# Kernel tuning notes

Measured on AMD Instinct MI355X. Metric: run time of the kernel, lower is better.

The kernel has to match this reference:

```python
import jax, jax.numpy as jnp
import numpy as np

N = 100000   # nodes
E = 1600000  # edges
F = 128      # num_features
NF = 4       # n_factor
D = 64       # n_dim = dim // n_factor = 256 // 4
NL = 3       # n_layer
G = 128      # num graphs in batch


def setup_inputs() -> dict:
    key = jax.random.key(0)
    ks = jax.random.split(key, 10)
    s = 0.05
    x = jax.random.normal(ks[0], (N, F), jnp.float32)
    edge_index = jax.random.randint(ks[1], (2, E), 0, N)
    att = jax.random.uniform(ks[2], (NF, E), jnp.float32)
    batch = jnp.sort(jax.random.randint(ks[3], (N,), 0, G))
    lin_W = jax.random.normal(ks[4], (NF, F, D), jnp.float32) * s
    lin_b = jnp.zeros((NF, D), jnp.float32)
    conv_Wrel = jax.random.normal(ks[5], (NF, NL, D, D), jnp.float32) * s
    conv_brel = jnp.zeros((NF, NL, D), jnp.float32)
    conv_Wroot = jax.random.normal(ks[6], (NF, NL, D, D), jnp.float32) * s
    gru_Wih = jax.random.normal(ks[7], (NF, 3 * D, D), jnp.float32) * s
    gru_Whh = jax.random.normal(ks[8], (NF, 3 * D, D), jnp.float32) * s
    gru_bih = jnp.zeros((NF, 3 * D), jnp.float32)
    gru_bhh = jnp.zeros((NF, 3 * D), jnp.float32)
    return dict(x=x, edge_index=edge_index, att=att, batch=batch,
                lin_W=lin_W, lin_b=lin_b,
                conv_Wrel=conv_Wrel, conv_brel=conv_brel, conv_Wroot=conv_Wroot,
                gru_Wih=gru_Wih, gru_Whh=gru_Whh, gru_bih=gru_bih, gru_bhh=gru_bhh,
                num_graphs=G)


def _gru_cell(xin, h, Wih, Whh, bih, bhh):
    # torch.nn.GRU single step: r,z,n gates
    gi = xin @ Wih.T + bih  # [N, 3D]
    gh = h @ Whh.T + bhh
    ir, iz, inn = jnp.split(gi, 3, axis=-1)
    hr, hz, hn = jnp.split(gh, 3, axis=-1)
    r = jax.nn.sigmoid(ir + hr)
    z = jax.nn.sigmoid(iz + hz)
    n = jnp.tanh(inn + r * hn)
    return (1.0 - z) * n + z * h


def reference(x, edge_index, att, batch, lin_W, lin_b, conv_Wrel, conv_brel,
              conv_Wroot, gru_Wih, gru_Whh, gru_bih, gru_bhh, num_graphs):
    src, dst = edge_index[0], edge_index[1]
    counts = jax.ops.segment_sum(jnp.ones((N,), x.dtype), batch, num_segments=num_graphs)
    counts = jnp.maximum(counts, 1.0)[:, None]
    outs, feats = [], []
    for f in range(NF):
        w = att[f][:, None]                       # [E,1] edge weights for this factor
        out = x @ lin_W[f] + lin_b[f]             # [N,D]
        h = out                                   # initial GRU hidden state
        for l in range(NL):
            # GraphConv: lin_rel(scatter_add(w * x_src -> dst)) + lin_root(x)
            agg = jax.ops.segment_sum(out[src] * w, dst, num_segments=N)
            m = jax.nn.relu(agg @ conv_Wrel[f, l] + conv_brel[f, l] + out @ conv_Wroot[f, l])
            h = _gru_cell(m, h, gru_Wih[f], gru_Whh[f], gru_bih[f], gru_bhh[f])
            out = h
        feats.append(out)
        # global mean pool
        outs.append(jax.ops.segment_sum(out, batch, num_segments=num_graphs) / counts)
    return (jnp.stack(outs), jnp.stack(feats))
```

## Files before the change

### kernel.cpp

```cpp
#include <hip/hip_runtime.h>

#define NN   100000
#define EE   1600000
#define FDIM 128
#define NFAC 4
#define DD   64
#define NLAY 3
#define GG   128
#define ROW  (NFAC * DD)

#define PF_STRIDE 57344
#define OFF_WREL  8192
#define OFF_WROOT 20480
#define OFF_WIH   32768
#define OFF_WHH   45056
#define PREP_TOTAL (NFAC * PF_STRIDE)

typedef __bf16 bf16x8_t __attribute__((ext_vector_type(8)));
typedef float  f32x4_t  __attribute__((ext_vector_type(4)));

__device__ __forceinline__ unsigned short f2bf(float x) {
    unsigned u = __float_as_uint(x);
    u += 0x7fffu + ((u >> 16) & 1u);
    return (unsigned short)(u >> 16);
}
__device__ __forceinline__ float b2f(unsigned short h) {
    return __uint_as_float(((unsigned)h) << 16);
}
__device__ __forceinline__ float sigm(float x) { return 1.f / (1.f + __expf(-x)); }
__device__ __forceinline__ float tanh_f(float x) {
    float t = __expf(-2.f * fabsf(x));
    float r = (1.f - t) / (1.f + t);
    return x >= 0.f ? r : -r;
}

__global__ __launch_bounds__(256) void k_init(int* deg, int* cursor, float* outs) {
    int i = blockIdx.x * 256 + threadIdx.x;
    if (i < NN) { deg[i] = 0; cursor[i] = 0; }
    if (i < NFAC * GG * DD) outs[i] = 0.f;
}

__global__ __launch_bounds__(256) void k_prep(const float* x, const float* linW,
                                              const float* wrel, const float* wroot,
                                              const float* wih, const float* whh,
                                              unsigned short* x16, unsigned short* prep) {
    for (int i = blockIdx.x * 256 + threadIdx.x; i < NN * FDIM; i += gridDim.x * 256)
        x16[i] = f2bf(x[i]);
    for (int idx = blockIdx.x * 256 + threadIdx.x; idx < PREP_TOTAL; idx += gridDim.x * 256) {
        int f = idx / PF_STRIDE, r = idx % PF_STRIDE;
        int e, KB, mode, l = 0;
        if (r < OFF_WREL)       { e = r;                 KB = 4; mode = 0; }
        else if (r < OFF_WROOT) { int rr = r - OFF_WREL;  l = rr >> 12; e = rr & 4095; KB = 2; mode = 1; }
        else if (r < OFF_WIH)   { int rr = r - OFF_WROOT; l = rr >> 12; e = rr & 4095; KB = 2; mode = 2; }
        else if (r < OFF_WHH)   { e = r - OFF_WIH;        KB = 2; mode = 3; }
        else                    { e = r - OFF_WHH;        KB = 2; mode = 4; }
        int j = e & 7, lane = (e >> 3) & 63, t = e >> 9;
        int kb = t % KB, nt = t / KB;
        int k = kb * 32 + (lane >> 4) * 8 + j;
        int n = nt * 16 + (lane & 15);
        float v;
        if (mode == 0)      v = linW[(f * FDIM + k) * DD + n];
        else if (mode == 1) v = wrel[((f * 3 + l) * DD + k) * DD + n];
        else if (mode == 2) v = wroot[((f * 3 + l) * DD + k) * DD + n];
        else if (mode == 3) v = wih[(f * 192 + n) * DD + k];
        else                v = whh[(f * 192 + n) * DD + k];
        prep[idx] = f2bf(v);
    }
}

__global__ __launch_bounds__(256) void k_count(const int* batch, float* counts) {
    __shared__ int lb[GG + 1];
    int t = threadIdx.x;
    if (t <= GG) {
        int lo = 0, hi = NN;
        while (lo < hi) { int mid = (lo + hi) >> 1; if (batch[mid] < t) lo = mid + 1; else hi = mid; }
        lb[t] = lo;
    }
    __syncthreads();
    if (t < GG) counts[t] = (float)(lb[t + 1] - lb[t]);
}

__global__ __launch_bounds__(256) void k_deg(const int* ei, int* deg) {
    int e = blockIdx.x * 256 + threadIdx.x;
    if (e < EE) atomicAdd(&deg[ei[EE + e]], 1);
}
__global__ __launch_bounds__(256) void k_scan1(const int* deg, int* row_pos, int* bsum) {
    __shared__ int lds[256];
    int tid = threadIdx.x, idx = blockIdx.x * 256 + tid;
    int v = (idx < NN) ? deg[idx] : 0;
    lds[tid] = v; __syncthreads();
    for (int s = 1; s < 256; s <<= 1) {
        int t = (tid >= s) ? lds[tid - s] : 0;
        __syncthreads();
        lds[tid] += t;
        __syncthreads();
    }
    if (idx < NN) row_pos[idx] = lds[tid] - v;
    if (tid == 255) bsum[blockIdx.x] = lds[255];
}
__global__ __launch_bounds__(512) void k_scan2(int* bsum) {
    __shared__ int lds[512];
    int tid = threadIdx.x;
    int v = (tid < 391) ? bsum[tid] : 0;
    lds[tid] = v; __syncthreads();
    for (int s = 1; s < 512; s <<= 1) {
        int t = (tid >= s) ? lds[tid - s] : 0;
        __syncthreads();
        lds[tid] += t;
        __syncthreads();
    }
    bsum[tid] = lds[tid] - v;
}
__global__ __launch_bounds__(256) void k_rowptr(const int* row_pos, const int* boff, int* row_ptr) {
    int i = blockIdx.x * 256 + threadIdx.x;
    if (i < NN) row_ptr[i] = row_pos[i] + boff[i >> 8];
    if (i == 0) row_ptr[NN] = EE;
}
__global__ __launch_bounds__(256) void k_fill(const int* ei, const float* att,
                                              const int* row_ptr, int* cursor,
                                              int* csr_src, float* csr_att) {
    int e = blockIdx.x * 256 + threadIdx.x;
    if (e >= EE) return;
    int d = ei[EE + e];
    int slot = row_ptr[d] + atomicAdd(&cursor[d], 1);
    csr_src[slot] = ei[e];
    *(float4*)(csr_att + (size_t)slot * 4) =
        make_float4(att[e], att[EE + e], att[2 * EE + e], att[3 * EE + e]);
}

__global__ __launch_bounds__(256) void k_lin(const unsigned short* x16, const unsigned short* prep,
                                             const float* linb, unsigned short* out16) {
    int n0 = blockIdx.x * 64;
    __shared__ unsigned short xs[64 * 136];
    int tid = threadIdx.x;
    for (int t = tid; t < 1024; t += 256) {
        int row = t >> 4, seg = t & 15;
        int gn = n0 + row; if (gn >= NN) gn = NN - 1;
        *(uint4*)(xs + row * 136 + seg * 8) = *(const uint4*)(x16 + (size_t)gn * FDIM + seg * 8);
    }
    __syncthreads();
    int w = tid >> 6, lane = tid & 63, mrow = lane & 15, q = lane >> 4;
    const unsigned short* wp = prep + w * PF_STRIDE;
    for (int mt = 0; mt < 4; mt++) {
        bf16x8_t a[4];
#pragma unroll
        for (int kb = 0; kb < 4; kb++)
            a[kb] = *(const bf16x8_t*)(xs + (mt * 16 + mrow) * 136 + kb * 32 + q * 8);
#pragma unroll
        for (int nt = 0; nt < 4; nt++) {
            f32x4_t acc = {0.f, 0.f, 0.f, 0.f};
#pragma unroll
            for (int kb = 0; kb < 4; kb++) {
                bf16x8_t b = *(const bf16x8_t*)(wp + ((nt * 4 + kb) * 64 + lane) * 8);
                acc = __builtin_amdgcn_mfma_f32_16x16x32_bf16(a[kb], b, acc, 0, 0, 0);
            }
            int col = nt * 16 + mrow;
            float bias = linb[w * DD + col];
#pragma unroll
            for (int r = 0; r < 4; r++) {
                int node = n0 + mt * 16 + q * 4 + r;
                if (node < NN) out16[(size_t)node * ROW + w * DD + col] = f2bf(acc[r] + bias);
            }
        }
    }
}

__global__ __launch_bounds__(256) void k_gather(const int* row_ptr, const int* csr_src, const float* csr_att,
                                                const unsigned short* out16, unsigned short* agg16) {
    int wave = threadIdx.x >> 6, lane = threadIdx.x & 63;
    int n = blockIdx.x * 4 + wave;
    if (n >= NN) return;
    int row = row_ptr[n], end = row_ptr[n + 1];
    int total = end - row;
    int fsel = lane >> 4, loff = lane * 4;
    float a0 = 0.f, a1 = 0.f, a2 = 0.f, a3 = 0.f;
    for (int base = 0; base < total; base += 16) {
        int s[16]; float w[16];
#pragma unroll
        for (int j = 0; j < 16; j++) {
            int e = base + j;
            int idx = row + (e < total ? e : total - 1);
            s[j] = csr_src[idx];
            float ww = csr_att[(size_t)idx * 4 + fsel];
            w[j] = (e < total) ? ww : 0.f;
        }
        uint2 v[16];
#pragma unroll
        for (int j = 0; j < 16; j++)
            v[j] = *(const uint2*)(out16 + (size_t)s[j] * ROW + loff);
#pragma unroll
        for (int j = 0; j < 16; j++) {
            a0 = fmaf(w[j], __uint_as_float(v[j].x << 16), a0);
            a1 = fmaf(w[j], __uint_as_float(v[j].x & 0xffff0000u), a1);
            a2 = fmaf(w[j], __uint_as_float(v[j].y << 16), a2);
            a3 = fmaf(w[j], __uint_as_float(v[j].y & 0xffff0000u), a3);
        }
    }
    ushort4 r;
    r.x = f2bf(a0); r.y = f2bf(a1); r.z = f2bf(a2); r.w = f2bf(a3);
    *(ushort4*)(agg16 + (size_t)n * ROW + loff) = r;
}

__global__ __launch_bounds__(256) void k_layer(int l, const unsigned short* agg16, unsigned short* out16,
                                               const unsigned short* prep, const float* brel,
                                               const float* bih, const float* bhh,
                                               float* feats, int last) {
    int f = blockIdx.y, n0 = blockIdx.x * 64;
    __shared__ unsigned short A1[64 * 72];
    __shared__ unsigned short A2[64 * 72];
    __shared__ unsigned short Mt[64 * 72];
    int tid = threadIdx.x;
    for (int t = tid; t < 512; t += 256) {
        int row = t >> 3, seg = t & 7;
        int gn = n0 + row; if (gn >= NN) gn = NN - 1;
        *(uint4*)(A1 + row * 72 + seg * 8) = *(const uint4*)(agg16 + (size_t)gn * ROW + f * DD + seg * 8);
        *(uint4*)(A2 + row * 72 + seg * 8) = *(const uint4*)(out16 + (size_t)gn * ROW + f * DD + seg * 8);
    }
    __syncthreads();
    int w = tid >> 6, lane = tid & 63, mrow = lane & 15, q = lane >> 4;
    const unsigned short* wrel  = prep + f * PF_STRIDE + OFF_WREL  + l * 4096;
    const unsigned short* wroot = prep + f * PF_STRIDE + OFF_WROOT + l * 4096;

#pragma unroll
    for (int nt = 0; nt < 4; nt++) {
        f32x4_t acc = {0.f, 0.f, 0.f, 0.f};
#pragma unroll
        for (int kb = 0; kb < 2; kb++) {
            bf16x8_t a1 = *(const bf16x8_t*)(A1 + (w * 16 + mrow) * 72 + kb * 32 + q * 8);
            bf16x8_t b1 = *(const bf16x8_t*)(wrel + ((nt * 2 + kb) * 64 + lane) * 8);
            acc = __builtin_amdgcn_mfma_f32_16x16x32_bf16(a1, b1, acc, 0, 0, 0);
            bf16x8_t a2 = *(const bf16x8_t*)(A2 + (w * 16 + mrow) * 72 + kb * 32 + q * 8);
            bf16x8_t b2 = *(const bf16x8_t*)(wroot + ((nt * 2 + kb) * 64 + lane) * 8);
            acc = __builtin_amdgcn_mfma_f32_16x16x32_bf16(a2, b2, acc, 0, 0, 0);
        }
        int col = nt * 16 + mrow;
        float bias = brel[(f * 3 + l) * DD + col];
#pragma unroll
        for (int r = 0; r < 4; r++) {
            float mv = acc[r] + bias;
            mv = mv > 0.f ? mv : 0.f;
            Mt[(w * 16 + q * 4 + r) * 72 + col] = f2bf(mv);
        }
    }
    __syncthreads();

    const unsigned short* wih = prep + f * PF_STRIDE + OFF_WIH;
    const unsigned short* whh = prep + f * PF_STRIDE + OFF_WHH;
#pragma unroll
    for (int nt = 0; nt < 4; nt++) {
        f32x4_t ir = {0.f,0.f,0.f,0.f}, iz = {0.f,0.f,0.f,0.f}, in_ = {0.f,0.f,0.f,0.f};
        f32x4_t hr = {0.f,0.f,0.f,0.f}, hz = {0.f,0.f,0.f,0.f}, hn  = {0.f,0.f,0.f,0.f};
#pragma unroll
        for (int kb = 0; kb < 2; kb++) {
            bf16x8_t am = *(const bf16x8_t*)(Mt + (w * 16 + mrow) * 72 + kb * 32 + q * 8);
            bf16x8_t ah = *(const bf16x8_t*)(A2 + (w * 16 + mrow) * 72 + kb * 32 + q * 8);
            bf16x8_t br = *(const bf16x8_t*)(wih + (((nt)     * 2 + kb) * 64 + lane) * 8);
            bf16x8_t bz = *(const bf16x8_t*)(wih + (((nt + 4) * 2 + kb) * 64 + lane) * 8);
            bf16x8_t bn = *(const bf16x8_t*)(wih + (((nt + 8) * 2 + kb) * 64 + lane) * 8);
            ir = __builtin_amdgcn_mfma_f32_16x16x32_bf16(am, br, ir, 0, 0, 0);
            iz = __builtin_amdgcn_mfma_f32_16x16x32_bf16(am, bz, iz, 0, 0, 0);
            in_ = __builtin_amdgcn_mfma_f32_16x16x32_bf16(am, bn, in_, 0, 0, 0);
            bf16x8_t cr = *(const bf16x8_t*)(whh + (((nt)     * 2 + kb) * 64 + lane) * 8);
            bf16x8_t cz = *(const bf16x8_t*)(whh + (((nt + 4) * 2 + kb) * 64 + lane) * 8);
            bf16x8_t cn = *(const bf16x8_t*)(whh + (((nt + 8) * 2 + kb) * 64 + lane) * 8);
            hr = __builtin_amdgcn_mfma_f32_16x16x32_bf16(ah, cr, hr, 0, 0, 0);
            hz = __builtin_amdgcn_mfma_f32_16x16x32_bf16(ah, cz, hz, 0, 0, 0);
            hn = __builtin_amdgcn_mfma_f32_16x16x32_bf16(ah, cn, hn, 0, 0, 0);
        }
        int col = nt * 16 + mrow;
        float bi_r = bih[f * 192 + col],        bh_r = bhh[f * 192 + col];
        float bi_z = bih[f * 192 + 64 + col],   bh_z = bhh[f * 192 + 64 + col];
        float bi_n = bih[f * 192 + 128 + col],  bh_n = bhh[f * 192 + 128 + col];
#pragma unroll
        for (int r = 0; r < 4; r++) {
            float rg = sigm(ir[r] + bi_r + hr[r] + bh_r);
            float z  = sigm(iz[r] + bi_z + hz[r] + bh_z);
            float nn = tanh_f(in_[r] + bi_n + rg * (hn[r] + bh_n));
            float h  = b2f(A2[(w * 16 + q * 4 + r) * 72 + col]);
            float hp = (1.f - z) * nn + z * h;
            int node = n0 + w * 16 + q * 4 + r;
            if (node < NN) {
                out16[(size_t)node * ROW + f * DD + col] = f2bf(hp);
                if (last) feats[((size_t)f * NN + node) * DD + col] = hp;
            }
        }
    }
}

__global__ __launch_bounds__(256) void k_pool(const float* feats, const int* batch, float* outs) {
    int f = blockIdx.y, w = threadIdx.x >> 6, lane = threadIdx.x & 63;
    int nbase = blockIdx.x * 256 + w * 64;
    if (nbase >= NN) return;
    int g_cur = batch[nbase];
    float acc = 0.f;
    for (int i = 0; i < 64; i++) {
        int n = nbase + i;
        if (n >= NN) break;
        int g = batch[n];
        float v = feats[((size_t)f * NN + n) * DD + lane];
        if (g != g_cur) {
            atomicAdd(&outs[(f * GG + g_cur) * DD + lane], acc);
            acc = v; g_cur = g;
        } else acc += v;
    }
    atomicAdd(&outs[(f * GG + g_cur) * DD + lane], acc);
}
__global__ __launch_bounds__(256) void k_norm(float* outs, const float* counts) {
    int i = blockIdx.x * 256 + threadIdx.x;
    if (i < NFAC * GG * DD) {
        int g = (i >> 6) & (GG - 1);
        outs[i] /= fmaxf(counts[g], 1.f);
    }
}

extern "C" void kernel_launch(void* const* d_in, const int* in_sizes, int n_in,
                              void* d_out, int out_size, void* d_ws, size_t ws_size,
                              hipStream_t stream) {
    const float* x    = (const float*)d_in[0];
    const int*   ei   = (const int*)d_in[1];
    const float* att  = (const float*)d_in[2];
    const int*   batch= (const int*)d_in[3];
    const float* linW = (const float*)d_in[4];
    const float* linb = (const float*)d_in[5];
    const float* wrel = (const float*)d_in[6];
    const float* brel = (const float*)d_in[7];
    const float* wroot= (const float*)d_in[8];
    const float* wih  = (const float*)d_in[9];
    const float* whh  = (const float*)d_in[10];
    const float* bih  = (const float*)d_in[11];
    const float* bhh  = (const float*)d_in[12];

    float* outs  = (float*)d_out;
    float* feats = (float*)d_out + NFAC * GG * DD;

    char* p = (char*)d_ws;
    unsigned short* out16 = (unsigned short*)p; p += (size_t)NN * ROW * 2;
    unsigned short* agg16 = (unsigned short*)p; p += (size_t)NN * ROW * 2;
    unsigned short* x16   = (unsigned short*)p; p += (size_t)NN * FDIM * 2;
    unsigned short* prep  = (unsigned short*)p; p += (size_t)PREP_TOTAL * 2;
    float* csr_att        = (float*)p;          p += (size_t)EE * 16;
    int* csr_src          = (int*)p;            p += (size_t)EE * 4;
    int* deg              = (int*)p;            p += (size_t)NN * 4;
    int* cursor           = (int*)p;            p += (size_t)NN * 4;
    int* row_pos          = (int*)p;            p += (size_t)NN * 4;
    int* row_ptr          = (int*)p;            p += (size_t)(NN + 1) * 4;
    int* boff             = (int*)p;            p += 512 * 4;
    float* counts         = (float*)p;          p += 512;

    k_init  <<<dim3(391),  dim3(256), 0, stream>>>(deg, cursor, outs);
    k_prep  <<<dim3(4096), dim3(256), 0, stream>>>(x, linW, wrel, wroot, wih, whh, x16, prep);
    k_count <<<dim3(1),    dim3(256), 0, stream>>>(batch, counts);
    k_deg   <<<dim3(6250), dim3(256), 0, stream>>>(ei, deg);
    k_scan1 <<<dim3(391),  dim3(256), 0, stream>>>(deg, row_pos, boff);
    k_scan2 <<<dim3(1),    dim3(512), 0, stream>>>(boff);
    k_rowptr<<<dim3(391),  dim3(256), 0, stream>>>(row_pos, boff, row_ptr);
    k_fill  <<<dim3(6250), dim3(256), 0, stream>>>(ei, att, row_ptr, cursor, csr_src, csr_att);
    k_lin   <<<dim3(1563), dim3(256), 0, stream>>>(x16, prep, linb, out16);
    for (int l = 0; l < NLAY; l++) {
        k_gather<<<dim3(25000),   dim3(256), 0, stream>>>(row_ptr, csr_src, csr_att, out16, agg16);
        k_layer <<<dim3(1563, 4), dim3(256), 0, stream>>>(l, agg16, out16, prep, brel, bih, bhh,
                                                          feats, (l == NLAY - 1) ? 1 : 0);
    }
    k_pool <<<dim3(391, 4), dim3(256), 0, stream>>>(feats, batch, outs);
    k_norm <<<dim3(128),    dim3(256), 0, stream>>>(outs, counts);
}
```

Baseline: 1.104 ms.

## Keep weight fragments in registers across row tiles and shrink gather batch

```diff
diff --git a/kernel.cpp b/kernel.cpp
--- a/kernel.cpp
+++ b/kernel.cpp
@@ -141,21 +141,26 @@
     __syncthreads();
     int w = tid >> 6, lane = tid & 63, mrow = lane & 15, q = lane >> 4;
     const unsigned short* wp = prep + w * PF_STRIDE;
-    for (int mt = 0; mt < 4; mt++) {
-        bf16x8_t a[4];
+    bf16x8_t a[4][4];
+#pragma unroll
+    for (int mt = 0; mt < 4; mt++)
 #pragma unroll
         for (int kb = 0; kb < 4; kb++)
-            a[kb] = *(const bf16x8_t*)(xs + (mt * 16 + mrow) * 136 + kb * 32 + q * 8);
-#pragma unroll
-        for (int nt = 0; nt < 4; nt++) {
+            a[mt][kb] = *(const bf16x8_t*)(xs + (mt * 16 + mrow) * 136 + kb * 32 + q * 8);
+#pragma unroll
+    for (int nt = 0; nt < 4; nt++) {
+        bf16x8_t b[4];
+#pragma unroll
+        for (int kb = 0; kb < 4; kb++)
+            b[kb] = *(const bf16x8_t*)(wp + ((nt * 4 + kb) * 64 + lane) * 8);
+        int col = nt * 16 + mrow;
+        float bias = linb[w * DD + col];
+#pragma unroll
+        for (int mt = 0; mt < 4; mt++) {
             f32x4_t acc = {0.f, 0.f, 0.f, 0.f};
 #pragma unroll
-            for (int kb = 0; kb < 4; kb++) {
-                bf16x8_t b = *(const bf16x8_t*)(wp + ((nt * 4 + kb) * 64 + lane) * 8);
-                acc = __builtin_amdgcn_mfma_f32_16x16x32_bf16(a[kb], b, acc, 0, 0, 0);
-            }
-            int col = nt * 16 + mrow;
-            float bias = linb[w * DD + col];
+            for (int kb = 0; kb < 4; kb++)
+                acc = __builtin_amdgcn_mfma_f32_16x16x32_bf16(a[mt][kb], b[kb], acc, 0, 0, 0);
 #pragma unroll
             for (int r = 0; r < 4; r++) {
                 int node = n0 + mt * 16 + q * 4 + r;
@@ -174,22 +179,22 @@
     int total = end - row;
     int fsel = lane >> 4, loff = lane * 4;
     float a0 = 0.f, a1 = 0.f, a2 = 0.f, a3 = 0.f;
-    for (int base = 0; base < total; base += 16) {
-        int s[16]; float w[16];
-#pragma unroll
-        for (int j = 0; j < 16; j++) {
+    for (int base = 0; base < total; base += 8) {
+        int s[8]; float w[8];
+#pragma unroll
+        for (int j = 0; j < 8; j++) {
             int e = base + j;
             int idx = row + (e < total ? e : total - 1);
             s[j] = csr_src[idx];
             float ww = csr_att[(size_t)idx * 4 + fsel];
             w[j] = (e < total) ? ww : 0.f;
         }
-        uint2 v[16];
-#pragma unroll
-        for (int j = 0; j < 16; j++)
+        uint2 v[8];
+#pragma unroll
+        for (int j = 0; j < 8; j++)
             v[j] = *(const uint2*)(out16 + (size_t)s[j] * ROW + loff);
 #pragma unroll
-        for (int j = 0; j < 16; j++) {
+        for (int j = 0; j < 8; j++) {
             a0 = fmaf(w[j], __uint_as_float(v[j].x << 16), a0);
             a1 = fmaf(w[j], __uint_as_float(v[j].x & 0xffff0000u), a1);
             a2 = fmaf(w[j], __uint_as_float(v[j].y << 16), a2);
@@ -221,64 +226,74 @@
     const unsigned short* wrel  = prep + f * PF_STRIDE + OFF_WREL  + l * 4096;
     const unsigned short* wroot = prep + f * PF_STRIDE + OFF_WROOT + l * 4096;
 
-#pragma unroll
-    for (int nt = 0; nt < 4; nt++) {
-        f32x4_t acc = {0.f, 0.f, 0.f, 0.f};
+    {
+        bf16x8_t wr1[2], wr2[2];
 #pragma unroll
         for (int kb = 0; kb < 2; kb++) {
-            bf16x8_t a1 = *(const bf16x8_t*)(A1 + (w * 16 + mrow) * 72 + kb * 32 + q * 8);
-            bf16x8_t b1 = *(const bf16x8_t*)(wrel + ((nt * 2 + kb) * 64 + lane) * 8);
-            acc = __builtin_amdgcn_mfma_f32_16x16x32_bf16(a1, b1, acc, 0, 0, 0);
-            bf16x8_t a2 = *(const bf16x8_t*)(A2 + (w * 16 + mrow) * 72 + kb * 32 + q * 8);
-            bf16x8_t b2 = *(const bf16x8_t*)(wroot + ((nt * 2 + kb) * 64 + lane) * 8);
-            acc = __builtin_amdgcn_mfma_f32_16x16x32_bf16(a2, b2, acc, 0, 0, 0);
-        }
-        int col = nt * 16 + mrow;
+            wr1[kb] = *(const bf16x8_t*)(wrel  + ((w * 2 + kb) * 64 + lane) * 8);
+            wr2[kb] = *(const bf16x8_t*)(wroot + ((w * 2 + kb) * 64 + lane) * 8);
+        }
+        int col = w * 16 + mrow;
         float bias = brel[(f * 3 + l) * DD + col];
 #pragma unroll
-        for (int r = 0; r < 4; r++) {
-            float mv = acc[r] + bias;
-            mv = mv > 0.f ? mv : 0.f;
-            Mt[(w * 16 + q * 4 + r) * 72 + col] = f2bf(mv);
+        for (int mt = 0; mt < 4; mt++) {
+            f32x4_t acc = {0.f, 0.f, 0.f, 0.f};
+#pragma unroll
+            for (int kb = 0; kb < 2; kb++) {
+                bf16x8_t a1 = *(const bf16x8_t*)(A1 + (mt * 16 + mrow) * 72 + kb * 32 + q * 8);
+                acc = __builtin_amdgcn_mfma_f32_16x16x32_bf16(a1, wr1[kb], acc, 0, 0, 0);
+                bf16x8_t a2 = *(const bf16x8_t*)(A2 + (mt * 16 + mrow) * 72 + kb * 32 + q * 8);
+                acc = __builtin_amdgcn_mfma_f32_16x16x32_bf16(a2, wr2[kb], acc, 0, 0, 0);
+            }
+#pragma unroll
+            for (int r = 0; r < 4; r++) {
+                float mv = acc[r] + bias;
+                mv = mv > 0.f ? mv : 0.f;
+                Mt[(mt * 16 + q * 4 + r) * 72 + col] = f2bf(mv);
+            }
         }
     }
     __syncthreads();
 
     const unsigned short* wih = prep + f * PF_STRIDE + OFF_WIH;
     const unsigned short* whh = prep + f * PF_STRIDE + OFF_WHH;
-#pragma unroll
-    for (int nt = 0; nt < 4; nt++) {
+    bf16x8_t Br[2], Bz[2], Bn[2], Cr[2], Cz[2], Cn[2];
+#pragma unroll
+    for (int kb = 0; kb < 2; kb++) {
+        Br[kb] = *(const bf16x8_t*)(wih + (((w)     * 2 + kb) * 64 + lane) * 8);
+        Bz[kb] = *(const bf16x8_t*)(wih + (((w + 4) * 2 + kb) * 64 + lane) * 8);
+        Bn[kb] = *(const bf16x8_t*)(wih + (((w + 8) * 2 + kb) * 64 + lane) * 8);
+        Cr[kb] = *(const bf16x8_t*)(whh + (((w)     * 2 + kb) * 64 + lane) * 8);
+        Cz[kb] = *(const bf16x8_t*)(whh + (((w + 4) * 2 + kb) * 64 + lane) * 8);
+        Cn[kb] = *(const bf16x8_t*)(whh + (((w + 8) * 2 + kb) * 64 + lane) * 8);
+    }
+    int col = w * 16 + mrow;
+    float bi_r = bih[f * 192 + col],        bh_r = bhh[f * 192 + col];
+    float bi_z = bih[f * 192 + 64 + col],   bh_z = bhh[f * 192 + 64 + col];
+    float bi_n = bih[f * 192 + 128 + col],  bh_n = bhh[f * 192 + 128 + col];
+#pragma unroll
+    for (int mt = 0; mt < 4; mt++) {
         f32x4_t ir = {0.f,0.f,0.f,0.f}, iz = {0.f,0.f,0.f,0.f}, in_ = {0.f,0.f,0.f,0.f};
         f32x4_t hr = {0.f,0.f,0.f,0.f}, hz = {0.f,0.f,0.f,0.f}, hn  = {0.f,0.f,0.f,0.f};
 #pragma unroll
         for (int kb = 0; kb < 2; kb++) {
-            bf16x8_t am = *(const bf16x8_t*)(Mt + (w * 16 + mrow) * 72 + kb * 32 + q * 8);
-            bf16x8_t ah = *(const bf16x8_t*)(A2 + (w * 16 + mrow) * 72 + kb * 32 + q * 8);
-            bf16x8_t br = *(const bf16x8_t*)(wih + (((nt)     * 2 + kb) * 64 + lane) * 8);
-            bf16x8_t bz = *(const bf16x8_t*)(wih + (((nt + 4) * 2 + kb) * 64 + lane) * 8);
-            bf16x8_t bn = *(const bf16x8_t*)(wih + (((nt + 8) * 2 + kb) * 64 + lane) * 8);
-            ir = __builtin_amdgcn_mfma_f32_16x16x32_bf16(am, br, ir, 0, 0, 0);
-            iz = __builtin_amdgcn_mfma_f32_16x16x32_bf16(am, bz, iz, 0, 0, 0);
-            in_ = __builtin_amdgcn_mfma_f32_16x16x32_bf16(am, bn, in_, 0, 0, 0);
-            bf16x8_t cr = *(const bf16x8_t*)(whh + (((nt)     * 2 + kb) * 64 + lane) * 8);
-            bf16x8_t cz = *(const bf16x8_t*)(whh + (((nt + 4) * 2 + kb) * 64 + lane) * 8);
-            bf16x8_t cn = *(const bf16x8_t*)(whh + (((nt + 8) * 2 + kb) * 64 + lane) * 8);
-            hr = __builtin_amdgcn_mfma_f32_16x16x32_bf16(ah, cr, hr, 0, 0, 0);
-            hz = __builtin_amdgcn_mfma_f32_16x16x32_bf16(ah, cz, hz, 0, 0, 0);
-            hn = __builtin_amdgcn_mfma_f32_16x16x32_bf16(ah, cn, hn, 0, 0, 0);
-        }
-        int col = nt * 16 + mrow;
-        float bi_r = bih[f * 192 + col],        bh_r = bhh[f * 192 + col];
-        float bi_z = bih[f * 192 + 64 + col],   bh_z = bhh[f * 192 + 64 + col];
-        float bi_n = bih[f * 192 + 128 + col],  bh_n = bhh[f * 192 + 128 + col];
+            bf16x8_t am = *(const bf16x8_t*)(Mt + (mt * 16 + mrow) * 72 + kb * 32 + q * 8);
+            bf16x8_t ah = *(const bf16x8_t*)(A2 + (mt * 16 + mrow) * 72 + kb * 32 + q * 8);
+            ir  = __builtin_amdgcn_mfma_f32_16x16x32_bf16(am, Br[kb], ir, 0, 0, 0);
+            iz  = __builtin_amdgcn_mfma_f32_16x16x32_bf16(am, Bz[kb], iz, 0, 0, 0);
+            in_ = __builtin_amdgcn_mfma_f32_16x16x32_bf16(am, Bn[kb], in_, 0, 0, 0);
+            hr  = __builtin_amdgcn_mfma_f32_16x16x32_bf16(ah, Cr[kb], hr, 0, 0, 0);
+            hz  = __builtin_amdgcn_mfma_f32_16x16x32_bf16(ah, Cz[kb], hz, 0, 0, 0);
+            hn  = __builtin_amdgcn_mfma_f32_16x16x32_bf16(ah, Cn[kb], hn, 0, 0, 0);
+        }
 #pragma unroll
         for (int r = 0; r < 4; r++) {
             float rg = sigm(ir[r] + bi_r + hr[r] + bh_r);
             float z  = sigm(iz[r] + bi_z + hz[r] + bh_z);
             float nn = tanh_f(in_[r] + bi_n + rg * (hn[r] + bh_n));
-            float h  = b2f(A2[(w * 16 + q * 4 + r) * 72 + col]);
+            float h  = b2f(A2[(mt * 16 + q * 4 + r) * 72 + col]);
             float hp = (1.f - z) * nn + z * h;
-            int node = n0 + w * 16 + q * 4 + r;
+            int node = n0 + mt * 16 + q * 4 + r;
             if (node < NN) {
                 out16[(size_t)node * ROW + f * DD + col] = f2bf(hp);
                 if (last) feats[((size_t)f * NN + node) * DD + col] = hp;
```

Result: faster. 998.7 us (-9.5%).
